# Performance work log

Measured on AMD Instinct MI355X. Metric: run time of the kernel, lower is better.

## Reference

```python
import jax, jax.numpy as jnp
import numpy as np

N = 50000        # nodes
E_RAND = 800000  # random edges (self-loops appended)
H = 4            # heads
F_IN, D1, D2 = 128, 64, 64
MLP_H, NCLS = 200, 2
NEG_SLOPE = 0.2
EPS = 1e-5


def setup_inputs() -> dict:
    key = jax.random.key(0)
    ks = jax.random.split(key, 18)
    p = lambda k, shape: (jax.random.normal(k, shape, jnp.float32) * 0.05)
    features = jax.random.normal(ks[0], (N, F_IN), jnp.float32)
    loops = jnp.arange(N, dtype=jnp.int32)
    src = jnp.concatenate([jax.random.randint(ks[1], (E_RAND,), 0, N, jnp.int32), loops])
    dst = jnp.concatenate([jax.random.randint(ks[2], (E_RAND,), 0, N, jnp.int32), loops])
    return {
        "features": features, "src": src, "dst": dst,
        "W1": p(ks[3], (F_IN, H * D1)), "al1": p(ks[4], (H, D1)), "ar1": p(ks[5], (H, D1)), "b1": p(ks[6], (H * D1,)),
        "W2": p(ks[7], (D1, H * D2)), "al2": p(ks[8], (H, D2)), "ar2": p(ks[9], (H, D2)), "b2": p(ks[10], (H * D2,)),
        "Wm1": p(ks[11], (D2, MLP_H)), "bm1": p(ks[12], (MLP_H,)),
        "gamma": jnp.ones((MLP_H,), jnp.float32), "beta": jnp.zeros((MLP_H,), jnp.float32),
        "Wm2": p(ks[13], (MLP_H, NCLS)), "bm2": p(ks[14], (NCLS,)),
    }


def gat_layer(x, W, al, ar, b, src, dst):
    # x: [N, F]; W: [F, H*D]
    Hh, D = al.shape
    h = (x @ W).reshape(N, Hh, D)                      # [N,H,D]
    el = jnp.einsum('nhd,hd->nh', h, al)               # [N,H]
    er = jnp.einsum('nhd,hd->nh', h, ar)               # [N,H]
    e = jax.nn.leaky_relu(el[src] + er[dst], NEG_SLOPE)  # [E,H]
    # edge softmax over incoming edges of each dst node
    m = jax.ops.segment_max(e, dst, num_segments=N)    # [N,H]
    ex = jnp.exp(e - m[dst])
    s = jax.ops.segment_sum(ex, dst, num_segments=N)   # [N,H]
    a = ex / s[dst]                                    # [E,H]
    out = jax.ops.segment_sum(a[:, :, None] * h[src], dst, num_segments=N)  # [N,H,D]
    out = jax.nn.relu(out + b.reshape(1, Hh, D))
    return out.mean(axis=1)                            # mean over heads -> [N,D]


def reference(features, src, dst, W1, al1, ar1, b1, W2, al2, ar2, b2,
              Wm1, bm1, gamma, beta, Wm2, bm2):
    h = gat_layer(features, W1, al1, ar1, b1, src, dst)   # dropout = identity (eval)
    h = gat_layer(h, W2, al2, ar2, b2, src, dst)
    # MLPPredictor: Dropout(id) -> Linear -> ReLU -> BatchNorm1d (batch stats) -> Linear
    z = jax.nn.relu(h @ Wm1 + bm1)                        # [N, MLP_H]
    mu = z.mean(axis=0)
    var = ((z - mu) ** 2).mean(axis=0)                    # biased var (torch BN)
    z = (z - mu) * jax.lax.rsqrt(var + EPS) * gamma + beta
    return z @ Wm2 + bm2                                  # [N, NCLS]
```

## Files before the change

kernel.cpp:

```cpp
#include <hip/hip_runtime.h>
#include <hip/hip_bf16.h>

#define NNODES 50000
#define MLP_HID 200
#define NB_SCAN 196
#define CAP 128

#define NB_W1   256
#define NB_W2   256
#define NB_ZC   196
#define INIT_BLOCKS (NB_W1 + NB_W2 + NB_ZC + 1)

typedef __attribute__((ext_vector_type(8))) short bf16x8;
typedef __attribute__((ext_vector_type(4))) float f32x4;

__device__ __forceinline__ unsigned short f2bf(float x){
    unsigned u = __float_as_uint(x);
    unsigned r = (u + 0x7fffu + ((u >> 16) & 1u)) >> 16;
    return (unsigned short)r;
}
__device__ __forceinline__ float bflo(unsigned u){ return __uint_as_float(u << 16); }
__device__ __forceinline__ float bfhi(unsigned u){ return __uint_as_float(u & 0xffff0000u); }

__global__ __launch_bounds__(256) void init_all(
    const float* __restrict__ W1, unsigned short* __restrict__ W1T,
    const float* __restrict__ W2, unsigned short* __restrict__ W2T,
    int* __restrict__ cnt, float* __restrict__ bn_acc )
{
    const int b = blockIdx.x, tid = threadIdx.x;
    if (b < NB_W1){
        int c = b;
        if (tid < 128) W1T[(size_t)c * 128 + tid] = f2bf(W1[(size_t)tid * 256 + c]);
    } else if (b < NB_W1 + NB_W2){
        int c = b - NB_W1;
        if (tid < 64) W2T[(size_t)c * 64 + tid] = f2bf(W2[(size_t)tid * 256 + c]);
    } else if (b < NB_W1 + NB_W2 + NB_ZC){
        int i = (b - NB_W1 - NB_W2) * 256 + tid;
        if (i < NNODES) cnt[i] = 0;
    } else {
        if (tid < 2 * MLP_HID - 256) bn_acc[256 + tid] = 0.f;
        bn_acc[tid] = 0.f;
    }
}

template<int K, bool F32IN>
__global__ __launch_bounds__(256) void mfma_gemm_attn(
    const void* __restrict__ Aptr,
    const unsigned short* __restrict__ WT,
    const float* __restrict__ al, const float* __restrict__ ar,
    unsigned short* __restrict__ hb,
    float* __restrict__ el, float* __restrict__ er, int M)
{
    const int wv = threadIdx.x >> 6, lane = threadIdx.x & 63;
    const int r0 = blockIdx.x * 64 + wv * 16;
    const int l15 = lane & 15, ks = lane >> 4;

    f32x4 acc[16];
    #pragma unroll
    for (int nt = 0; nt < 16; nt++)
        #pragma unroll
        for (int q = 0; q < 4; q++) acc[nt][q] = 0.f;

    const int arow = min(r0 + l15, M - 1);
    const unsigned short* aptr_b = (const unsigned short*)Aptr + (size_t)arow * K + ks * 8;
    const float*          aptr_f = (const float*)Aptr          + (size_t)arow * K + ks * 8;
    const unsigned short* bptr = WT + (size_t)l15 * K + ks * 8;

    #pragma unroll
    for (int k0 = 0; k0 < K; k0 += 32){
        bf16x8 a;
        if (F32IN){
            float4 f0 = *(const float4*)(aptr_f + k0);
            float4 f1 = *(const float4*)(aptr_f + k0 + 4);
            a[0] = (short)f2bf(f0.x); a[1] = (short)f2bf(f0.y);
            a[2] = (short)f2bf(f0.z); a[3] = (short)f2bf(f0.w);
            a[4] = (short)f2bf(f1.x); a[5] = (short)f2bf(f1.y);
            a[6] = (short)f2bf(f1.z); a[7] = (short)f2bf(f1.w);
        } else {
            a = *(const bf16x8*)(aptr_b + k0);
        }
        #pragma unroll
        for (int nt = 0; nt < 16; nt++){
            bf16x8 b = *(const bf16x8*)(bptr + (size_t)nt * 16 * K + k0);
            acc[nt] = __builtin_amdgcn_mfma_f32_16x16x32_bf16(a, b, acc[nt], 0, 0, 0);
        }
    }

    float elv[4][4], erv[4][4];
    #pragma unroll
    for (int r = 0; r < 4; r++)
        #pragma unroll
        for (int hh = 0; hh < 4; hh++){ elv[r][hh] = 0.f; erv[r][hh] = 0.f; }

    #pragma unroll
    for (int nt = 0; nt < 16; nt++){
        int col = nt * 16 + l15;
        float alv = al[col], arv = ar[col];
        #pragma unroll
        for (int reg = 0; reg < 4; reg++){
            elv[reg][nt >> 2] = fmaf(acc[nt][reg], alv, elv[reg][nt >> 2]);
            erv[reg][nt >> 2] = fmaf(acc[nt][reg], arv, erv[reg][nt >> 2]);
        }
    }
    #pragma unroll
    for (int o = 8; o > 0; o >>= 1){
        #pragma unroll
        for (int reg = 0; reg < 4; reg++)
            #pragma unroll
            for (int hh = 0; hh < 4; hh++){
                elv[reg][hh] += __shfl_xor(elv[reg][hh], o);
                erv[reg][hh] += __shfl_xor(erv[reg][hh], o);
            }
    }
    if (l15 == 0){
        #pragma unroll
        for (int reg = 0; reg < 4; reg++){
            int r = r0 + ks * 4 + reg;
            if (r < M){
                #pragma unroll
                for (int hh = 0; hh < 4; hh++){
                    el[r * 4 + hh] = elv[reg][hh];
                    er[r * 4 + hh] = erv[reg][hh];
                }
            }
        }
    }

    __shared__ __align__(16) unsigned short hbuf[4][16][264];
    #pragma unroll
    for (int nt = 0; nt < 16; nt++)
        #pragma unroll
        for (int reg = 0; reg < 4; reg++)
            hbuf[wv][ks * 4 + reg][nt * 16 + l15] = f2bf(acc[nt][reg]);
    #pragma unroll
    for (int t = 0; t < 8; t++){
        int chunk = t * 64 + lane;
        int rr = chunk >> 5;
        int cc = (chunk & 31) * 8;
        int r = r0 + rr;
        if (r < M){
            uint4 v = *(const uint4*)&hbuf[wv][rr][cc];
            *(uint4*)&hb[(size_t)r * 256 + cc] = v;
        }
    }
}

template<int KT, bool RELU, bool BN>
__global__ __launch_bounds__(256) void gemm_tile(const float* __restrict__ A,
                                                 const float* __restrict__ B,
                                                 const float* __restrict__ bias,
                                                 float* __restrict__ C,
                                                 float* __restrict__ bn_sum,
                                                 float* __restrict__ bn_sumsq,
                                                 int M, int Nc){
    __shared__ float As[16][64];
    __shared__ float Bs[16][64];
    __shared__ float bnred[16][64];
    const int tid = threadIdx.x;
    const int tx = tid & 15, ty = tid >> 4;
    const int r0 = blockIdx.y * 64, c0 = blockIdx.x * 64;
    float acc[4][4] = {};
    const int lr  = tid >> 2,  lk4 = (tid & 3) * 4;
    const int bk  = tid >> 4,  bc4 = (tid & 15) * 4;

    for (int k0 = 0; k0 < KT; k0 += 16){
        float4 av = make_float4(0.f,0.f,0.f,0.f);
        if (r0 + lr < M) av = *(const float4*)&A[(size_t)(r0 + lr) * KT + k0 + lk4];
        As[lk4+0][lr] = av.x; As[lk4+1][lr] = av.y;
        As[lk4+2][lr] = av.z; As[lk4+3][lr] = av.w;

        if (c0 + bc4 + 3 < Nc){
            float4 bv = *(const float4*)&B[(size_t)(k0 + bk) * Nc + c0 + bc4];
            Bs[bk][bc4+0] = bv.x; Bs[bk][bc4+1] = bv.y;
            Bs[bk][bc4+2] = bv.z; Bs[bk][bc4+3] = bv.w;
        } else {
            #pragma unroll
            for (int j = 0; j < 4; j++){
                int c = c0 + bc4 + j;
                Bs[bk][bc4+j] = (c < Nc) ? B[(size_t)(k0 + bk) * Nc + c] : 0.f;
            }
        }
        __syncthreads();
        #pragma unroll
        for (int kk = 0; kk < 16; kk++){
            float4 a = *(const float4*)&As[kk][ty*4];
            float4 b = *(const float4*)&Bs[kk][tx*4];
            float arr[4] = {a.x,a.y,a.z,a.w};
            float brr[4] = {b.x,b.y,b.z,b.w};
            #pragma unroll
            for (int i = 0; i < 4; i++)
                #pragma unroll
                for (int j = 0; j < 4; j++)
                    acc[i][j] = fmaf(arr[i], brr[j], acc[i][j]);
        }
        __syncthreads();
    }

    float cs[4] = {0,0,0,0}, css[4] = {0,0,0,0};
    #pragma unroll
    for (int i = 0; i < 4; i++){
        int r = r0 + ty*4 + i;
        bool rok = r < M;
        #pragma unroll
        for (int j = 0; j < 4; j++){
            int c = c0 + tx*4 + j;
            if (c >= Nc) continue;
            float v = acc[i][j];
            if (bias) v += bias[c];
            if (RELU) v = fmaxf(v, 0.f);
            if (rok){
                C[(size_t)r * Nc + c] = v;
                if (BN){ cs[j] += v; css[j] += v * v; }
            }
        }
    }
    if (BN){
        #pragma unroll
        for (int j = 0; j < 4; j++) bnred[ty][tx*4+j] = cs[j];
        __syncthreads();
        if (tid < 64){
            float s = 0.f;
            #pragma unroll
            for (int t = 0; t < 16; t++) s += bnred[t][tid];
            if (c0 + tid < Nc) atomicAdd(&bn_sum[c0 + tid], s);
        }
        __syncthreads();
        #pragma unroll
        for (int j = 0; j < 4; j++) bnred[ty][tx*4+j] = css[j];
        __syncthreads();
        if (tid < 64){
            float s = 0.f;
            #pragma unroll
            for (int t = 0; t < 16; t++) s += bnred[t][tid];
            if (c0 + tid < Nc) atomicAdd(&bn_sumsq[c0 + tid], s);
        }
    }
}

__global__ __launch_bounds__(256) void csr_count(const int* __restrict__ dst,
                                                 int* __restrict__ cnt, int E){
    int e = blockIdx.x * blockDim.x + threadIdx.x;
    if (e < E) atomicAdd(&cnt[dst[e]], 1);
}

__global__ __launch_bounds__(256) void csr_bsum(const int* __restrict__ cnt,
                                                int* __restrict__ bsum){
    __shared__ int red[256];
    int i = blockIdx.x * 256 + threadIdx.x;
    red[threadIdx.x] = (i < NNODES) ? cnt[i] : 0;
    __syncthreads();
    for (int off = 128; off > 0; off >>= 1){
        if (threadIdx.x < off) red[threadIdx.x] += red[threadIdx.x + off];
        __syncthreads();
    }
    if (threadIdx.x == 0) bsum[blockIdx.x] = red[0];
}

__global__ __launch_bounds__(256) void csr_bscan(const int* __restrict__ bsum,
                                                 int* __restrict__ boff){
    __shared__ int part[256];
    int t = threadIdx.x;
    int v = (t < NB_SCAN) ? bsum[t] : 0;
    part[t] = v;
    __syncthreads();
    for (int off = 1; off < 256; off <<= 1){
        int u = (t >= off) ? part[t - off] : 0;
        __syncthreads();
        part[t] += u;
        __syncthreads();
    }
    if (t < NB_SCAN) boff[t] = part[t] - v;
}

__global__ __launch_bounds__(256) void csr_fill(const int* __restrict__ cnt,
                                                const int* __restrict__ boff,
                                                int* __restrict__ row_ptr,
                                                int* __restrict__ cursor){
    __shared__ int part[256];
    int b = blockIdx.x, t = threadIdx.x;
    int i = b * 256 + t;
    int c = (i < NNODES) ? cnt[i] : 0;
    part[t] = c;
    __syncthreads();
    for (int off = 1; off < 256; off <<= 1){
        int u = (t >= off) ? part[t - off] : 0;
        __syncthreads();
        part[t] += u;
        __syncthreads();
    }
    int excl = part[t] - c + boff[b];
    if (i < NNODES){ row_ptr[i] = excl; cursor[i] = excl; }
    if (i == NNODES - 1) row_ptr[NNODES] = excl + c;
}

__global__ __launch_bounds__(256) void csr_scatter(const int* __restrict__ src,
                                                   const int* __restrict__ dst,
                                                   int* __restrict__ cursor,
                                                   int* __restrict__ col_src, int E){
    int e = blockIdx.x * blockDim.x + threadIdx.x;
    if (e >= E) return;
    int pos = atomicAdd(&cursor[dst[e]], 1);
    col_src[pos] = src[e];
}

__global__ __launch_bounds__(256) void gat_edge_v7(
    const int* __restrict__ row_ptr, const int* __restrict__ col_src,
    const float* __restrict__ el, const float* __restrict__ er,
    const unsigned short* __restrict__ hb, const float* __restrict__ bias,
    float* __restrict__ out_f, unsigned short* __restrict__ out_b, int N)
{
    __shared__ float s_w[4][4][132];
    __shared__ int   s_idx[4][CAP];

    const int wv = threadIdx.x >> 6;
    const int lane = threadIdx.x & 63;
    const int n = blockIdx.x * 4 + wv;
    if (n >= N) return;

    const int rs = row_ptr[n], re = row_ptr[n + 1];
    const int K = re - rs;
    const float4 ern = *(const float4*)&er[n * 4];
    float (*sw)[132] = s_w[wv];
    int* sidx = s_idx[wv];

    float ls0 = 0.f, ls1 = 0.f, ls2 = 0.f, ls3 = 0.f;
    for (int k = lane; k < K; k += 64){
        int s = col_src[rs + k];
        float4 e4 = *(const float4*)&el[s * 4];
        float e0 = e4.x + ern.x; e0 = (e0 >= 0.f) ? e0 : 0.2f * e0;
        float e1 = e4.y + ern.y; e1 = (e1 >= 0.f) ? e1 : 0.2f * e1;
        float e2 = e4.z + ern.z; e2 = (e2 >= 0.f) ? e2 : 0.2f * e2;
        float e3 = e4.w + ern.w; e3 = (e3 >= 0.f) ? e3 : 0.2f * e3;
        float w0 = __expf(e0), w1 = __expf(e1), w2 = __expf(e2), w3 = __expf(e3);
        if (k < CAP){
            sidx[k] = s;
            sw[0][k] = w0; sw[1][k] = w1; sw[2][k] = w2; sw[3][k] = w3;
        }
        ls0 += w0; ls1 += w1; ls2 += w2; ls3 += w3;
    }
    #pragma unroll
    for (int o = 32; o > 0; o >>= 1){
        ls0 += __shfl_xor(ls0, o); ls1 += __shfl_xor(ls1, o);
        ls2 += __shfl_xor(ls2, o); ls3 += __shfl_xor(ls3, o);
    }
    const int slot = lane >> 5;
    const int c8   = (lane & 31) * 8;
    const int hc   = c8 >> 6;
    const float invh = 1.f / (hc == 0 ? ls0 : hc == 1 ? ls1 : hc == 2 ? ls2 : ls3);

    float acc[8];
    #pragma unroll
    for (int q = 0; q < 8; q++) acc[q] = 0.f;

    for (int base = 0; base < K; base += CAP){
        if (base > 0){
            for (int k = base + lane; k < min(K, base + CAP); k += 64){
                int s = col_src[rs + k];
                float4 e4 = *(const float4*)&el[s * 4];
                float e0 = e4.x + ern.x; e0 = (e0 >= 0.f) ? e0 : 0.2f * e0;
                float e1 = e4.y + ern.y; e1 = (e1 >= 0.f) ? e1 : 0.2f * e1;
                float e2 = e4.z + ern.z; e2 = (e2 >= 0.f) ? e2 : 0.2f * e2;
                float e3 = e4.w + ern.w; e3 = (e3 >= 0.f) ? e3 : 0.2f * e3;
                int kk = k - base;
                sidx[kk] = s;
                sw[0][kk] = __expf(e0); sw[1][kk] = __expf(e1);
                sw[2][kk] = __expf(e2); sw[3][kk] = __expf(e3);
            }
        }
        const int rem = min(CAP, K - base);
        for (int j = slot; j < rem; j += 8){
            int   j1 = j + 2, j2 = j + 4, j3 = j + 6;
            int   jc1 = min(j1, rem - 1), jc2 = min(j2, rem - 1), jc3 = min(j3, rem - 1);
            float w0v = sw[hc][j];
            float w1v = (j1 < rem) ? sw[hc][j1] : 0.f;
            float w2v = (j2 < rem) ? sw[hc][j2] : 0.f;
            float w3v = (j3 < rem) ? sw[hc][j3] : 0.f;
            int   s0 = sidx[j], s1 = sidx[jc1], s2 = sidx[jc2], s3 = sidx[jc3];
            uint4 v0 = *(const uint4*)&hb[(size_t)s0 * 256 + c8];
            uint4 v1 = *(const uint4*)&hb[(size_t)s1 * 256 + c8];
            uint4 v2 = *(const uint4*)&hb[(size_t)s2 * 256 + c8];
            uint4 v3 = *(const uint4*)&hb[(size_t)s3 * 256 + c8];
            acc[0] = fmaf(w0v, bflo(v0.x), acc[0]); acc[1] = fmaf(w0v, bfhi(v0.x), acc[1]);
            acc[2] = fmaf(w0v, bflo(v0.y), acc[2]); acc[3] = fmaf(w0v, bfhi(v0.y), acc[3]);
            acc[4] = fmaf(w0v, bflo(v0.z), acc[4]); acc[5] = fmaf(w0v, bfhi(v0.z), acc[5]);
            acc[6] = fmaf(w0v, bflo(v0.w), acc[6]); acc[7] = fmaf(w0v, bfhi(v0.w), acc[7]);
            acc[0] = fmaf(w1v, bflo(v1.x), acc[0]); acc[1] = fmaf(w1v, bfhi(v1.x), acc[1]);
            acc[2] = fmaf(w1v, bflo(v1.y), acc[2]); acc[3] = fmaf(w1v, bfhi(v1.y), acc[3]);
            acc[4] = fmaf(w1v, bflo(v1.z), acc[4]); acc[5] = fmaf(w1v, bfhi(v1.z), acc[5]);
            acc[6] = fmaf(w1v, bflo(v1.w), acc[6]); acc[7] = fmaf(w1v, bfhi(v1.w), acc[7]);
            acc[0] = fmaf(w2v, bflo(v2.x), acc[0]); acc[1] = fmaf(w2v, bfhi(v2.x), acc[1]);
            acc[2] = fmaf(w2v, bflo(v2.y), acc[2]); acc[3] = fmaf(w2v, bfhi(v2.y), acc[3]);
            acc[4] = fmaf(w2v, bflo(v2.z), acc[4]); acc[5] = fmaf(w2v, bfhi(v2.z), acc[5]);
            acc[6] = fmaf(w2v, bflo(v2.w), acc[6]); acc[7] = fmaf(w2v, bfhi(v2.w), acc[7]);
            acc[0] = fmaf(w3v, bflo(v3.x), acc[0]); acc[1] = fmaf(w3v, bfhi(v3.x), acc[1]);
            acc[2] = fmaf(w3v, bflo(v3.y), acc[2]); acc[3] = fmaf(w3v, bfhi(v3.y), acc[3]);
            acc[4] = fmaf(w3v, bflo(v3.z), acc[4]); acc[5] = fmaf(w3v, bfhi(v3.z), acc[5]);
            acc[6] = fmaf(w3v, bflo(v3.w), acc[6]); acc[7] = fmaf(w3v, bfhi(v3.w), acc[7]);
        }
    }

    #pragma unroll
    for (int q = 0; q < 8; q++){
        acc[q] *= invh;
        acc[q] += __shfl_xor(acc[q], 32);
        acc[q] = fmaxf(acc[q] + bias[c8 + q], 0.f);
        acc[q] += __shfl_xor(acc[q], 8);
        acc[q] += __shfl_xor(acc[q], 16);
        acc[q] *= 0.25f;
    }
    if (lane < 8){
        uint4 pb;
        pb.x = (unsigned)f2bf(acc[0]) | ((unsigned)f2bf(acc[1]) << 16);
        pb.y = (unsigned)f2bf(acc[2]) | ((unsigned)f2bf(acc[3]) << 16);
        pb.z = (unsigned)f2bf(acc[4]) | ((unsigned)f2bf(acc[5]) << 16);
        pb.w = (unsigned)f2bf(acc[6]) | ((unsigned)f2bf(acc[7]) << 16);
        *(uint4*)&out_b[(size_t)n * 64 + lane * 8] = pb;
        if (out_f){
            *(float4*)&out_f[(size_t)n * 64 + lane * 8]     = make_float4(acc[0], acc[1], acc[2], acc[3]);
            *(float4*)&out_f[(size_t)n * 64 + lane * 8 + 4] = make_float4(acc[4], acc[5], acc[6], acc[7]);
        }
    }
}

__global__ __launch_bounds__(256) void mlp2(const float* __restrict__ z,
                                            const float* __restrict__ bn_sum,
                                            const float* __restrict__ bn_sumsq,
                                            const float* __restrict__ gamma,
                                            const float* __restrict__ beta,
                                            const float* __restrict__ Wm2,
                                            const float* __restrict__ bm2,
                                            float* __restrict__ out,
                                            int Nrows){
    __shared__ float s_scale[MLP_HID], s_shift[MLP_HID];
    const int tid = threadIdx.x;
    if (tid < MLP_HID){
        float inv = 1.f / (float)Nrows;
        float mu = bn_sum[tid] * inv;
        float var = bn_sumsq[tid] * inv - mu * mu;
        float rstd = rsqrtf(var + 1e-5f);
        float sc = rstd * gamma[tid];
        s_scale[tid] = sc;
        s_shift[tid] = beta[tid] - mu * sc;
    }
    __syncthreads();
    int n = (blockIdx.x * 256 + tid) >> 6;
    if (n >= Nrows) return;
    int lane = tid & 63;
    float a0 = 0.f, a1 = 0.f;
    for (int k = lane; k < MLP_HID; k += 64){
        float zn = z[(size_t)n * MLP_HID + k] * s_scale[k] + s_shift[k];
        a0 = fmaf(zn, Wm2[k * 2 + 0], a0);
        a1 = fmaf(zn, Wm2[k * 2 + 1], a1);
    }
    #pragma unroll
    for (int o = 32; o > 0; o >>= 1){
        a0 += __shfl_xor(a0, o);
        a1 += __shfl_xor(a1, o);
    }
    if (lane == 0){
        out[n * 2 + 0] = a0 + bm2[0];
        out[n * 2 + 1] = a1 + bm2[1];
    }
}

extern "C" void kernel_launch(void* const* d_in, const int* in_sizes, int n_in,
                              void* d_out, int out_size, void* d_ws, size_t ws_size,
                              hipStream_t stream) {
    const float* feat  = (const float*)d_in[0];
    const int*   src   = (const int*)  d_in[1];
    const int*   dst   = (const int*)  d_in[2];
    const float* W1    = (const float*)d_in[3];
    const float* al1   = (const float*)d_in[4];
    const float* ar1   = (const float*)d_in[5];
    const float* b1    = (const float*)d_in[6];
    const float* W2    = (const float*)d_in[7];
    const float* al2   = (const float*)d_in[8];
    const float* ar2   = (const float*)d_in[9];
    const float* b2    = (const float*)d_in[10];
    const float* Wm1   = (const float*)d_in[11];
    const float* bm1   = (const float*)d_in[12];
    const float* gamma = (const float*)d_in[13];
    const float* beta  = (const float*)d_in[14];
    const float* Wm2   = (const float*)d_in[15];
    const float* bm2   = (const float*)d_in[16];
    const int E = in_sizes[1];
    float* out = (float*)d_out;

    unsigned short* h_bf   = (unsigned short*)d_ws;
    unsigned short* o1_bf  = h_bf   + (size_t)NNODES * 256;
    unsigned short* o2_bf  = o1_bf  + (size_t)NNODES * 64;
    unsigned short* W1T    = o2_bf  + (size_t)NNODES * 64;
    unsigned short* W2T    = W1T + 256 * 128;
    float* z      = (float*)(W2T + 256 * 64);
    float* out2_f = z      + (size_t)NNODES * MLP_HID;
    float* el     = out2_f + (size_t)NNODES * 64;
    float* er     = el     + (size_t)NNODES * 4;
    float* bn_sum   = er + (size_t)NNODES * 4;
    float* bn_sumsq = bn_sum + MLP_HID;
    int* cnt      = (int*)(bn_sumsq + MLP_HID);
    int* row_ptr  = cnt + NNODES;
    int* cursor   = row_ptr + NNODES + 1;
    int* bsum     = cursor + NNODES;
    int* boff     = bsum + 256;
    int* col_src  = boff + 256;

    const dim3 blk(256);
    const int eg = (E + 255) / 256;
    const int gb = (NNODES + 63) / 64;
    const int ng4 = (NNODES + 3) / 4;

    init_all<<<INIT_BLOCKS, blk, 0, stream>>>(W1, W1T, W2, W2T, cnt, bn_sum);

    csr_count<<<eg, blk, 0, stream>>>(dst, cnt, E);
    csr_bsum<<<NB_SCAN, blk, 0, stream>>>(cnt, bsum);
    csr_bscan<<<1, blk, 0, stream>>>(bsum, boff);
    csr_fill<<<NB_SCAN, blk, 0, stream>>>(cnt, boff, row_ptr, cursor);
    csr_scatter<<<eg, blk, 0, stream>>>(src, dst, cursor, col_src, E);

    mfma_gemm_attn<128, true><<<gb, blk, 0, stream>>>(feat, W1T, al1, ar1,
                                                      h_bf, el, er, NNODES);
    gat_edge_v7<<<ng4, blk, 0, stream>>>(row_ptr, col_src, el, er, h_bf, b1,
                                         nullptr, o1_bf, NNODES);

    mfma_gemm_attn<64, false><<<gb, blk, 0, stream>>>(o1_bf, W2T, al2, ar2,
                                                      h_bf, el, er, NNODES);
    gat_edge_v7<<<ng4, blk, 0, stream>>>(row_ptr, col_src, el, er, h_bf, b2,
                                         out2_f, o2_bf, NNODES);

    gemm_tile<64,true,true><<<dim3((MLP_HID + 63) / 64, gb), blk, 0, stream>>>(
        out2_f, Wm1, bm1, z, bn_sum, bn_sumsq, NNODES, MLP_HID);

    mlp2<<<(NNODES * 64 + 255) / 256, blk, 0, stream>>>(
        z, bn_sum, bn_sumsq, gamma, beta, Wm2, bm2, out, NNODES);
}
```

Baseline: 372.3 us.

## Replace fp32 MLP GEMM with bf16 MFMA kernel fed by bf16 GAT output

The first MLP linear layer moves from a scalar fp32 tiled GEMM to a bf16 MFMA kernel. It reads the existing bf16 layer-2 output and uses a Wm1 matrix that is transposed and padded once in the init kernel. The kernel fuses bias, ReLU and the BatchNorm sum and sum-of-squares reduction, with one atomic per column per block. Because the second GAT layer no longer writes an fp32 copy of its output, a full write and read of that buffer is avoided. In exchange the MLP input is rounded to bf16, which reduces precision.

```diff
diff --git a/kernel.cpp b/kernel.cpp
--- a/kernel.cpp
+++ b/kernel.cpp
@@ -8,8 +8,9 @@
 
 #define NB_W1   256
 #define NB_W2   256
+#define NB_WM1  208
 #define NB_ZC   196
-#define INIT_BLOCKS (NB_W1 + NB_W2 + NB_ZC + 1)
+#define INIT_BLOCKS (NB_W1 + NB_W2 + NB_WM1 + NB_ZC + 1)
 
 typedef __attribute__((ext_vector_type(8))) short bf16x8;
 typedef __attribute__((ext_vector_type(4))) float f32x4;
@@ -25,6 +26,7 @@
 __global__ __launch_bounds__(256) void init_all(
     const float* __restrict__ W1, unsigned short* __restrict__ W1T,
     const float* __restrict__ W2, unsigned short* __restrict__ W2T,
+    const float* __restrict__ Wm1, unsigned short* __restrict__ Wm1T,
     int* __restrict__ cnt, float* __restrict__ bn_acc )
 {
     const int b = blockIdx.x, tid = threadIdx.x;
@@ -34,8 +36,13 @@
     } else if (b < NB_W1 + NB_W2){
         int c = b - NB_W1;
         if (tid < 64) W2T[(size_t)c * 64 + tid] = f2bf(W2[(size_t)tid * 256 + c]);
-    } else if (b < NB_W1 + NB_W2 + NB_ZC){
-        int i = (b - NB_W1 - NB_W2) * 256 + tid;
+    } else if (b < NB_W1 + NB_W2 + NB_WM1){
+        int c = b - NB_W1 - NB_W2;
+        if (tid < 64)
+            Wm1T[(size_t)c * 64 + tid] =
+                (c < MLP_HID) ? f2bf(Wm1[(size_t)tid * MLP_HID + c]) : (unsigned short)0;
+    } else if (b < NB_W1 + NB_W2 + NB_WM1 + NB_ZC){
+        int i = (b - NB_W1 - NB_W2 - NB_WM1) * 256 + tid;
         if (i < NNODES) cnt[i] = 0;
     } else {
         if (tid < 2 * MLP_HID - 256) bn_acc[256 + tid] = 0.f;
@@ -43,7 +50,7 @@
     }
 }
 
-template<int K, bool F32IN>
+template<int K, bool F32IN, bool STOREH>
 __global__ __launch_bounds__(256) void mfma_gemm_attn(
     const void* __restrict__ Aptr,
     const unsigned short* __restrict__ WT,
@@ -126,114 +133,88 @@
         }
     }
 
-    __shared__ __align__(16) unsigned short hbuf[4][16][264];
-    #pragma unroll
-    for (int nt = 0; nt < 16; nt++)
-        #pragma unroll
-        for (int reg = 0; reg < 4; reg++)
-            hbuf[wv][ks * 4 + reg][nt * 16 + l15] = f2bf(acc[nt][reg]);
-    #pragma unroll
-    for (int t = 0; t < 8; t++){
-        int chunk = t * 64 + lane;
-        int rr = chunk >> 5;
-        int cc = (chunk & 31) * 8;
-        int r = r0 + rr;
-        if (r < M){
-            uint4 v = *(const uint4*)&hbuf[wv][rr][cc];
-            *(uint4*)&hb[(size_t)r * 256 + cc] = v;
-        }
-    }
-}
-
-template<int KT, bool RELU, bool BN>
-__global__ __launch_bounds__(256) void gemm_tile(const float* __restrict__ A,
-                                                 const float* __restrict__ B,
-                                                 const float* __restrict__ bias,
-                                                 float* __restrict__ C,
-                                                 float* __restrict__ bn_sum,
-                                                 float* __restrict__ bn_sumsq,
-                                                 int M, int Nc){
-    __shared__ float As[16][64];
-    __shared__ float Bs[16][64];
-    __shared__ float bnred[16][64];
-    const int tid = threadIdx.x;
-    const int tx = tid & 15, ty = tid >> 4;
-    const int r0 = blockIdx.y * 64, c0 = blockIdx.x * 64;
-    float acc[4][4] = {};
-    const int lr  = tid >> 2,  lk4 = (tid & 3) * 4;
-    const int bk  = tid >> 4,  bc4 = (tid & 15) * 4;
-
-    for (int k0 = 0; k0 < KT; k0 += 16){
-        float4 av = make_float4(0.f,0.f,0.f,0.f);
-        if (r0 + lr < M) av = *(const float4*)&A[(size_t)(r0 + lr) * KT + k0 + lk4];
-        As[lk4+0][lr] = av.x; As[lk4+1][lr] = av.y;
-        As[lk4+2][lr] = av.z; As[lk4+3][lr] = av.w;
-
-        if (c0 + bc4 + 3 < Nc){
-            float4 bv = *(const float4*)&B[(size_t)(k0 + bk) * Nc + c0 + bc4];
-            Bs[bk][bc4+0] = bv.x; Bs[bk][bc4+1] = bv.y;
-            Bs[bk][bc4+2] = bv.z; Bs[bk][bc4+3] = bv.w;
-        } else {
+    if constexpr (STOREH){
+        __shared__ __align__(16) unsigned short hbuf[4][16][264];
+        #pragma unroll
+        for (int nt = 0; nt < 16; nt++)
             #pragma unroll
-            for (int j = 0; j < 4; j++){
-                int c = c0 + bc4 + j;
-                Bs[bk][bc4+j] = (c < Nc) ? B[(size_t)(k0 + bk) * Nc + c] : 0.f;
+            for (int reg = 0; reg < 4; reg++)
+                hbuf[wv][ks * 4 + reg][nt * 16 + l15] = f2bf(acc[nt][reg]);
+        #pragma unroll
+        for (int t = 0; t < 8; t++){
+            int chunk = t * 64 + lane;
+            int rr = chunk >> 5;
+            int cc = (chunk & 31) * 8;
+            int r = r0 + rr;
+            if (r < M){
+                uint4 v = *(const uint4*)&hbuf[wv][rr][cc];
+                *(uint4*)&hb[(size_t)r * 256 + cc] = v;
             }
         }
-        __syncthreads();
-        #pragma unroll
-        for (int kk = 0; kk < 16; kk++){
-            float4 a = *(const float4*)&As[kk][ty*4];
-            float4 b = *(const float4*)&Bs[kk][tx*4];
-            float arr[4] = {a.x,a.y,a.z,a.w};
-            float brr[4] = {b.x,b.y,b.z,b.w};
-            #pragma unroll
-            for (int i = 0; i < 4; i++)
-                #pragma unroll
-                for (int j = 0; j < 4; j++)
-                    acc[i][j] = fmaf(arr[i], brr[j], acc[i][j]);
-        }
-        __syncthreads();
-    }
-
-    float cs[4] = {0,0,0,0}, css[4] = {0,0,0,0};
-    #pragma unroll
-    for (int i = 0; i < 4; i++){
-        int r = r0 + ty*4 + i;
-        bool rok = r < M;
-        #pragma unroll
-        for (int j = 0; j < 4; j++){
-            int c = c0 + tx*4 + j;
-            if (c >= Nc) continue;
-            float v = acc[i][j];
-            if (bias) v += bias[c];
-            if (RELU) v = fmaxf(v, 0.f);
-            if (rok){
-                C[(size_t)r * Nc + c] = v;
-                if (BN){ cs[j] += v; css[j] += v * v; }
-            }
-        }
-    }
-    if (BN){
-        #pragma unroll
-        for (int j = 0; j < 4; j++) bnred[ty][tx*4+j] = cs[j];
-        __syncthreads();
-        if (tid < 64){
-            float s = 0.f;
-            #pragma unroll
-            for (int t = 0; t < 16; t++) s += bnred[t][tid];
-            if (c0 + tid < Nc) atomicAdd(&bn_sum[c0 + tid], s);
-        }
-        __syncthreads();
-        #pragma unroll
-        for (int j = 0; j < 4; j++) bnred[ty][tx*4+j] = css[j];
-        __syncthreads();
-        if (tid < 64){
-            float s = 0.f;
-            #pragma unroll
-            for (int t = 0; t < 16; t++) s += bnred[t][tid];
-            if (c0 + tid < Nc) atomicAdd(&bn_sumsq[c0 + tid], s);
-        }
+    }
+}
+
+__global__ __launch_bounds__(256) void mfma_mlp(
+    const unsigned short* __restrict__ Abf,
+    const unsigned short* __restrict__ WT,
+    const float* __restrict__ bm1,
+    float* __restrict__ z,
+    float* __restrict__ bn_sum, float* __restrict__ bn_sumsq, int M)
+{
+    __shared__ float s_sum[4][208], s_ssq[4][208];
+    const int wv = threadIdx.x >> 6, lane = threadIdx.x & 63;
+    const int r0 = blockIdx.x * 64 + wv * 16;
+    const int l15 = lane & 15, ks = lane >> 4;
+
+    f32x4 acc[13];
+    #pragma unroll
+    for (int nt = 0; nt < 13; nt++)
+        #pragma unroll
+        for (int q = 0; q < 4; q++) acc[nt][q] = 0.f;
+
+    const int arow = min(r0 + l15, M - 1);
+    const unsigned short* aptr = Abf + (size_t)arow * 64 + ks * 8;
+    const unsigned short* bptr = WT + (size_t)l15 * 64 + ks * 8;
+
+    #pragma unroll
+    for (int k0 = 0; k0 < 64; k0 += 32){
+        bf16x8 a = *(const bf16x8*)(aptr + k0);
+        #pragma unroll
+        for (int nt = 0; nt < 13; nt++){
+            bf16x8 b = *(const bf16x8*)(bptr + (size_t)nt * 16 * 64 + k0);
+            acc[nt] = __builtin_amdgcn_mfma_f32_16x16x32_bf16(a, b, acc[nt], 0, 0, 0);
+        }
+    }
+
+    #pragma unroll
+    for (int nt = 0; nt < 13; nt++){
+        int col = nt * 16 + l15;
+        bool colok = col < MLP_HID;
+        float bias = colok ? bm1[col] : 0.f;
+        float cs = 0.f, css = 0.f;
+        #pragma unroll
+        for (int reg = 0; reg < 4; reg++){
+            int r = r0 + ks * 4 + reg;
+            float v = fmaxf(acc[nt][reg] + bias, 0.f);
+            bool ok = colok && (r < M);
+            if (ok) z[(size_t)r * MLP_HID + col] = v;
+            float vv = ok ? v : 0.f;
+            cs += vv; css += vv * vv;
+        }
+        cs  += __shfl_xor(cs, 16);  cs  += __shfl_xor(cs, 32);
+        css += __shfl_xor(css, 16); css += __shfl_xor(css, 32);
+        if (ks == 0 && colok){
+            s_sum[wv][col] = cs;
+            s_ssq[wv][col] = css;
+        }
+    }
+    __syncthreads();
+    if (threadIdx.x < MLP_HID){
+        int c = threadIdx.x;
+        float a = s_sum[0][c] + s_sum[1][c] + s_sum[2][c] + s_sum[3][c];
+        float b = s_ssq[0][c] + s_ssq[1][c] + s_ssq[2][c] + s_ssq[3][c];
+        atomicAdd(&bn_sum[c], a);
+        atomicAdd(&bn_sumsq[c], b);
     }
 }
 
@@ -307,7 +288,7 @@
     const int* __restrict__ row_ptr, const int* __restrict__ col_src,
     const float* __restrict__ el, const float* __restrict__ er,
     const unsigned short* __restrict__ hb, const float* __restrict__ bias,
-    float* __restrict__ out_f, unsigned short* __restrict__ out_b, int N)
+    unsigned short* __restrict__ out_b, int N)
 {
     __shared__ float s_w[4][4][132];
     __shared__ int   s_idx[4][CAP];
@@ -415,10 +396,6 @@
         pb.z = (unsigned)f2bf(acc[4]) | ((unsigned)f2bf(acc[5]) << 16);
         pb.w = (unsigned)f2bf(acc[6]) | ((unsigned)f2bf(acc[7]) << 16);
         *(uint4*)&out_b[(size_t)n * 64 + lane * 8] = pb;
-        if (out_f){
-            *(float4*)&out_f[(size_t)n * 64 + lane * 8]     = make_float4(acc[0], acc[1], acc[2], acc[3]);
-            *(float4*)&out_f[(size_t)n * 64 + lane * 8 + 4] = make_float4(acc[4], acc[5], acc[6], acc[7]);
-        }
     }
 }
 
@@ -491,9 +468,9 @@
     unsigned short* o2_bf  = o1_bf  + (size_t)NNODES * 64;
     unsigned short* W1T    = o2_bf  + (size_t)NNODES * 64;
     unsigned short* W2T    = W1T + 256 * 128;
-    float* z      = (float*)(W2T + 256 * 64);
-    float* out2_f = z      + (size_t)NNODES * MLP_HID;
-    float* el     = out2_f + (size_t)NNODES * 64;
+    unsigned short* Wm1T   = W2T + 256 * 64;
+    float* z      = (float*)(Wm1T + 208 * 64);
+    float* el     = z      + (size_t)NNODES * MLP_HID;
     float* er     = el     + (size_t)NNODES * 4;
     float* bn_sum   = er + (size_t)NNODES * 4;
     float* bn_sumsq = bn_sum + MLP_HID;
@@ -509,7 +486,8 @@
     const int gb = (NNODES + 63) / 64;
     const int ng4 = (NNODES + 3) / 4;
 
-    init_all<<<INIT_BLOCKS, blk, 0, stream>>>(W1, W1T, W2, W2T, cnt, bn_sum);
+    init_all<<<INIT_BLOCKS, blk, 0, stream>>>(W1, W1T, W2, W2T, Wm1, Wm1T,
+                                              cnt, bn_sum);
 
     csr_count<<<eg, blk, 0, stream>>>(dst, cnt, E);
     csr_bsum<<<NB_SCAN, blk, 0, stream>>>(cnt, bsum);
@@ -517,18 +495,17 @@
     csr_fill<<<NB_SCAN, blk, 0, stream>>>(cnt, boff, row_ptr, cursor);
     csr_scatter<<<eg, blk, 0, stream>>>(src, dst, cursor, col_src, E);
 
-    mfma_gemm_attn<128, true><<<gb, blk, 0, stream>>>(feat, W1T, al1, ar1,
-                                                      h_bf, el, er, NNODES);
+    mfma_gemm_attn<128, true, true><<<gb, blk, 0, stream>>>(
+        feat, W1T, al1, ar1, h_bf, el, er, NNODES);
     gat_edge_v7<<<ng4, blk, 0, stream>>>(row_ptr, col_src, el, er, h_bf, b1,
-                                         nullptr, o1_bf, NNODES);
-
-    mfma_gemm_attn<64, false><<<gb, blk, 0, stream>>>(o1_bf, W2T, al2, ar2,
-                                                      h_bf, el, er, NNODES);
+                                         o1_bf, NNODES);
+
+    mfma_gemm_attn<64, false, true><<<gb, blk, 0, stream>>>(
+        o1_bf, W2T, al2, ar2, h_bf, el, er, NNODES);
     gat_edge_v7<<<ng4, blk, 0, stream>>>(row_ptr, col_src, el, er, h_bf, b2,
-                                         out2_f, o2_bf, NNODES);
-
-    gemm_tile<64,true,true><<<dim3((MLP_HID + 63) / 64, gb), blk, 0, stream>>>(
-        out2_f, Wm1, bm1, z, bn_sum, bn_sumsq, NNODES, MLP_HID);
+                                         o2_bf, NNODES);
+
+    mfma_mlp<<<gb, blk, 0, stream>>>(o2_bf, Wm1T, bm1, z, bn_sum, bn_sumsq, NNODES);
 
     mlp2<<<(NNODES * 64 + 255) / 256, blk, 0, stream>>>(
         z, bn_sum, bn_sumsq, gamma, beta, Wm2, bm2, out, NNODES);
```

New measurement: 380.6 us. 2.2% more time.
